# Kernel optimization log

Measured on AMD Instinct MI355X. Metric: run time of the kernel, lower is better.

## Reference

```python
import jax, jax.numpy as jnp
import numpy as np
import math

N = 8192
IN_FEATURES = 512
OUT_FEATURES = 64
NEG_INF = -9e15

def setup_inputs() -> dict:
    key = jax.random.key(0)
    k1, k2, k3, k4 = jax.random.split(key, 4)
    inp = jax.random.normal(k1, (N, IN_FEATURES), dtype=jnp.float32)
    adj = jax.random.randint(k2, (N, N), 0, 2, dtype=jnp.int32)
    # xavier_uniform with gain=1.414 for [in, out] weights
    limit = 1.414 * math.sqrt(6.0 / (IN_FEATURES + OUT_FEATURES))
    kW = jax.random.uniform(k3, (IN_FEATURES, OUT_FEATURES), dtype=jnp.float32, minval=-limit, maxval=limit)
    vW = jax.random.uniform(k4, (IN_FEATURES, OUT_FEATURES), dtype=jnp.float32, minval=-limit, maxval=limit)
    return {"input": inp, "adj": adj, "kW": kW, "vW": vW}

def reference(input, adj, kW, vW):
    kh = input @ kW                      # [N, d]
    vh = input @ vW                      # [N, d]
    d = kh.shape[1]
    K = (kh @ kh.T) / jnp.sqrt(jnp.asarray(d, dtype=kh.dtype))  # [N, N]
    scores = jnp.where(adj > 0, K, jnp.asarray(NEG_INF, dtype=K.dtype))
    attention = jax.nn.softmax(scores, axis=1)
    # dropout is a no-op (p=0.0 / eval mode)
    h_prime = attention @ vh             # [N, d]
    return jax.nn.elu(h_prime)           # concat=True path
```

## Files before the change

kernel.cpp:

```cpp
#include <hip/hip_runtime.h>
#include <math.h>

typedef __bf16 bf16_t;
typedef __bf16 bf16x8 __attribute__((ext_vector_type(8)));
typedef float f32x4 __attribute__((ext_vector_type(4)));

#define NN 8192
#define L2E 1.44269504088896340736f
#define SMAX 45.0f
#define KSCALE 0.35355339059327373f
#define ACCW 66

__global__ __launch_bounds__(256) void proj_kernel(
    const float* __restrict__ input,
    const float* __restrict__ kW,
    const float* __restrict__ vW,
    bf16_t* __restrict__ khs_hi,
    bf16_t* __restrict__ khs_lo,
    bf16_t* __restrict__ vhT)
{
    __shared__ __align__(16) bf16_t WkH[64][136];
    __shared__ __align__(16) bf16_t WkL[64][136];
    __shared__ __align__(16) bf16_t WvH[64][136];
    __shared__ __align__(16) bf16_t WvL[64][136];

    const int tid   = threadIdx.x;
    const int wv    = tid >> 6;
    const int lane  = tid & 63;
    const int l15   = lane & 15;
    const int quad  = lane >> 4;
    const int rbase = blockIdx.x * 64 + wv * 16;

    f32x4 kacc[4] = {};
    f32x4 vacc[4] = {};

    for (int kk = 0; kk < 4; ++kk) {
        __syncthreads();
        #pragma unroll
        for (int i = 0; i < 32; ++i) {
            int idx = tid + i * 256;
            int kl  = idx >> 6;
            int n   = idx & 63;
            float wk  = kW[(kk * 128 + kl) * 64 + n];
            float wv2 = vW[(kk * 128 + kl) * 64 + n];
            bf16_t kh = (bf16_t)wk;
            bf16_t vh = (bf16_t)wv2;
            WkH[n][kl] = kh;  WkL[n][kl] = (bf16_t)(wk - (float)kh);
            WvH[n][kl] = vh;  WvL[n][kl] = (bf16_t)(wv2 - (float)vh);
        }
        __syncthreads();

        #pragma unroll
        for (int kc = 0; kc < 4; ++kc) {
            const float* ap = &input[(size_t)(rbase + l15) * 512 + kk * 128 + kc * 32 + quad * 8];
            f32x4 a0 = *(const f32x4*)ap;
            f32x4 a1 = *(const f32x4*)(ap + 4);
            bf16x8 ah, al;
            #pragma unroll
            for (int j = 0; j < 4; ++j) {
                bf16_t h0 = (bf16_t)a0[j], h1 = (bf16_t)a1[j];
                ah[j]     = h0;  al[j]     = (bf16_t)(a0[j] - (float)h0);
                ah[4 + j] = h1;  al[4 + j] = (bf16_t)(a1[j] - (float)h1);
            }
            #pragma unroll
            for (int nb = 0; nb < 4; ++nb) {
                bf16x8 bkh = *(const bf16x8*)&WkH[nb * 16 + l15][kc * 32 + quad * 8];
                bf16x8 bkl = *(const bf16x8*)&WkL[nb * 16 + l15][kc * 32 + quad * 8];
                bf16x8 bvh = *(const bf16x8*)&WvH[nb * 16 + l15][kc * 32 + quad * 8];
                bf16x8 bvl = *(const bf16x8*)&WvL[nb * 16 + l15][kc * 32 + quad * 8];
                kacc[nb] = __builtin_amdgcn_mfma_f32_16x16x32_bf16(ah, bkh, kacc[nb], 0, 0, 0);
                kacc[nb] = __builtin_amdgcn_mfma_f32_16x16x32_bf16(al, bkh, kacc[nb], 0, 0, 0);
                kacc[nb] = __builtin_amdgcn_mfma_f32_16x16x32_bf16(ah, bkl, kacc[nb], 0, 0, 0);
                vacc[nb] = __builtin_amdgcn_mfma_f32_16x16x32_bf16(ah, bvh, vacc[nb], 0, 0, 0);
                vacc[nb] = __builtin_amdgcn_mfma_f32_16x16x32_bf16(al, bvh, vacc[nb], 0, 0, 0);
                vacc[nb] = __builtin_amdgcn_mfma_f32_16x16x32_bf16(ah, bvl, vacc[nb], 0, 0, 0);
            }
        }
    }

    #pragma unroll
    for (int nb = 0; nb < 4; ++nb) {
        const int dcol = nb * 16 + l15;
        #pragma unroll
        for (int r = 0; r < 4; ++r) {
            float v  = kacc[nb][r] * KSCALE;
            bf16_t h = (bf16_t)v;
            khs_hi[(size_t)(rbase + quad * 4 + r) * 64 + dcol] = h;
            khs_lo[(size_t)(rbase + quad * 4 + r) * 64 + dcol] = (bf16_t)(v - (float)h);
        }
        union { bf16_t b[4]; uint2 u; } pk;
        #pragma unroll
        for (int r = 0; r < 4; ++r) pk.b[r] = (bf16_t)vacc[nb][r];
        *(uint2*)&vhT[(size_t)dcol * NN + rbase + quad * 4] = pk.u;
    }
}

__global__ void zero_acc(float* __restrict__ acc) {
    int i = blockIdx.x * blockDim.x + threadIdx.x;
    if (i < NN * ACCW) acc[i] = 0.f;
}

__global__ __launch_bounds__(512, 4) void attn_kernel(
    const int* __restrict__ adj,
    const bf16_t* __restrict__ khs_hi,
    const bf16_t* __restrict__ khs_lo,
    const bf16_t* __restrict__ vhT,
    float* __restrict__ acc)
{
    __shared__ __align__(16) float PlBuf[8 * 1152];

    const int tid   = threadIdx.x;
    const int w     = tid >> 6;
    const int lane  = tid & 63;
    const int l15   = lane & 15;
    const int quad  = lane >> 4;
    const int rb    = blockIdx.x >> 1;
    const int ch    = blockIdx.x & 1;
    const int qbase = rb * 16;
    const int colstart = ch * 4096 + w * 512;

    const bf16x8 qh0 = *(const bf16x8*)&khs_hi[(size_t)(qbase + l15) * 64 + quad * 8];
    const bf16x8 qh1 = *(const bf16x8*)&khs_hi[(size_t)(qbase + l15) * 64 + 32 + quad * 8];
    const bf16x8 ql0 = *(const bf16x8*)&khs_lo[(size_t)(qbase + l15) * 64 + quad * 8];
    const bf16x8 ql1 = *(const bf16x8*)&khs_lo[(size_t)(qbase + l15) * 64 + 32 + quad * 8];

    bf16x8 ones;
    #pragma unroll
    for (int j = 0; j < 8; ++j) ones[j] = (bf16_t)1.0f;

    f32x4 o0 = {}, o1 = {}, o2 = {}, o3 = {}, o4 = {};

    const int* aptr = adj + (size_t)(qbase + quad * 4) * NN + colstart + l15;

    int acur[8], anxt[8];
    #pragma unroll
    for (int r = 0; r < 4; ++r) {
        acur[2 * r]     = aptr[(size_t)r * NN];
        acur[2 * r + 1] = aptr[(size_t)r * NN + 16];
    }

    for (int t = 0; t < 16; ++t) {
        const int colbase = colstart + t * 32;
        float* Plw = &PlBuf[w * 1152 + (t & 1) * 576];

        const bf16_t* kph = khs_hi + (size_t)(colbase + l15) * 64 + quad * 8;
        bf16x8 bh00 = *(const bf16x8*)(kph);
        bf16x8 bh01 = *(const bf16x8*)(kph + 32);
        bf16x8 bh10 = *(const bf16x8*)(kph + 16 * 64);
        bf16x8 bh11 = *(const bf16x8*)(kph + 16 * 64 + 32);
        const bf16_t* vp = vhT + (size_t)l15 * NN + colbase + quad * 8;
        bf16x8 bv0 = *(const bf16x8*)(vp);
        bf16x8 bv1 = *(const bf16x8*)(vp + (size_t)16 * NN);
        bf16x8 bv2 = *(const bf16x8*)(vp + (size_t)32 * NN);
        bf16x8 bv3 = *(const bf16x8*)(vp + (size_t)48 * NN);

        const int cnx = ((t + 1) & 15) * 32;
        #pragma unroll
        for (int r = 0; r < 4; ++r) {
            anxt[2 * r]     = aptr[(size_t)r * NN + cnx];
            anxt[2 * r + 1] = aptr[(size_t)r * NN + cnx + 16];
        }

        f32x4 zz = {};
        f32x4 s0 = __builtin_amdgcn_mfma_f32_16x16x32_bf16(qh0, bh00, zz, 0, 0, 0);
        s0 = __builtin_amdgcn_mfma_f32_16x16x32_bf16(qh1, bh01, s0, 0, 0, 0);
        s0 = __builtin_amdgcn_mfma_f32_16x16x32_bf16(ql0, bh00, s0, 0, 0, 0);
        s0 = __builtin_amdgcn_mfma_f32_16x16x32_bf16(ql1, bh01, s0, 0, 0, 0);
        f32x4 s1 = __builtin_amdgcn_mfma_f32_16x16x32_bf16(qh0, bh10, zz, 0, 0, 0);
        s1 = __builtin_amdgcn_mfma_f32_16x16x32_bf16(qh1, bh11, s1, 0, 0, 0);
        s1 = __builtin_amdgcn_mfma_f32_16x16x32_bf16(ql0, bh10, s1, 0, 0, 0);
        s1 = __builtin_amdgcn_mfma_f32_16x16x32_bf16(ql1, bh11, s1, 0, 0, 0);

        #pragma unroll
        for (int r = 0; r < 4; ++r) {
            float p0 = acur[2 * r]     > 0 ? __builtin_amdgcn_exp2f((s0[r] - SMAX) * L2E) : 0.f;
            float p1 = acur[2 * r + 1] > 0 ? __builtin_amdgcn_exp2f((s1[r] - SMAX) * L2E) : 0.f;
            Plw[(quad * 4 + r) * 36 + l15]      = p0;
            Plw[(quad * 4 + r) * 36 + 16 + l15] = p1;
        }

        __asm__ __volatile__("s_waitcnt lgkmcnt(0)" ::: "memory");

        f32x4 pfa = *(const f32x4*)&Plw[l15 * 36 + quad * 8];
        f32x4 pfb = *(const f32x4*)&Plw[l15 * 36 + quad * 8 + 4];
        bf16x8 pa;
        #pragma unroll
        for (int j = 0; j < 4; ++j) { pa[j] = (bf16_t)pfa[j]; pa[4 + j] = (bf16_t)pfb[j]; }

        o0 = __builtin_amdgcn_mfma_f32_16x16x32_bf16(pa, bv0, o0, 0, 0, 0);
        o1 = __builtin_amdgcn_mfma_f32_16x16x32_bf16(pa, bv1, o1, 0, 0, 0);
        o2 = __builtin_amdgcn_mfma_f32_16x16x32_bf16(pa, bv2, o2, 0, 0, 0);
        o3 = __builtin_amdgcn_mfma_f32_16x16x32_bf16(pa, bv3, o3, 0, 0, 0);
        o4 = __builtin_amdgcn_mfma_f32_16x16x32_bf16(pa, ones, o4, 0, 0, 0);

        #pragma unroll
        for (int i = 0; i < 8; ++i) acur[i] = anxt[i];
    }

    float* M = PlBuf;
    #pragma unroll
    for (int s = 4; s >= 1; s >>= 1) {
        __syncthreads();
        if (w >= s && w < 2 * s) {
            float* base = M + (w - s) * 16 * 68;
            #pragma unroll
            for (int r = 0; r < 4; ++r) {
                const int row = quad * 4 + r;
                base[row * 68 + l15]      = o0[r];
                base[row * 68 + 16 + l15] = o1[r];
                base[row * 68 + 32 + l15] = o2[r];
                base[row * 68 + 48 + l15] = o3[r];
                if (l15 == 0) base[row * 68 + 64] = o4[r];
            }
        }
        __syncthreads();
        if (w < s) {
            float* base = M + w * 16 * 68;
            #pragma unroll
            for (int r = 0; r < 4; ++r) {
                const int row = quad * 4 + r;
                o0[r] += base[row * 68 + l15];
                o1[r] += base[row * 68 + 16 + l15];
                o2[r] += base[row * 68 + 32 + l15];
                o3[r] += base[row * 68 + 48 + l15];
                o4[r] += base[row * 68 + 64];
            }
        }
    }

    if (w == 0) {
        #pragma unroll
        for (int r = 0; r < 4; ++r) {
            const size_t row = (size_t)qbase + quad * 4 + r;
            atomicAdd(&acc[row * ACCW + l15],      o0[r]);
            atomicAdd(&acc[row * ACCW + 16 + l15], o1[r]);
            atomicAdd(&acc[row * ACCW + 32 + l15], o2[r]);
            atomicAdd(&acc[row * ACCW + 48 + l15], o3[r]);
            if (l15 == 0) atomicAdd(&acc[row * ACCW + 64], o4[r]);
        }
    }
}

__global__ void finalize(const float* __restrict__ acc, float* __restrict__ out) {
    int i = blockIdx.x * blockDim.x + threadIdx.x;
    int row = i >> 6, d = i & 63;
    float l = acc[(size_t)row * ACCW + 64];
    float v = acc[(size_t)row * ACCW + d] / (l > 0.f ? l : 1.f);
    out[i] = v > 0.f ? v : expm1f(v);
}

extern "C" void kernel_launch(void* const* d_in, const int* in_sizes, int n_in,
                              void* d_out, int out_size, void* d_ws, size_t ws_size,
                              hipStream_t stream) {
    const float* input = nullptr;
    const int*   adj   = nullptr;
    const float* kW    = nullptr;
    const float* vW    = nullptr;
    for (int i = 0; i < n_in; ++i) {
        if (in_sizes[i] == 8192 * 512)            input = (const float*)d_in[i];
        else if (in_sizes[i] == 512 * 64) {
            if (!kW) kW = (const float*)d_in[i]; else vW = (const float*)d_in[i];
        } else                                    adj = (const int*)d_in[i];
    }
    float* out = (float*)d_out;

    bf16_t* khs_hi = (bf16_t*)d_ws;
    bf16_t* khs_lo = khs_hi + (size_t)NN * 64;
    bf16_t* vhT    = khs_lo + (size_t)NN * 64;
    float*  acc    = (float*)((char*)d_ws + 3u * 1024 * 1024);

    zero_acc<<<(NN * ACCW + 255) / 256, 256, 0, stream>>>(acc);
    proj_kernel<<<128, 256, 0, stream>>>(input, kW, vW, khs_hi, khs_lo, vhT);
    attn_kernel<<<1024, 512, 0, stream>>>(adj, khs_hi, khs_lo, vhT, acc);
    finalize<<<(NN * 64) / 512, 512, 0, stream>>>(acc, out);
}
```

Measured before the change: 519.1 us.

## Pre-pack adjacency into bitmask and read bits in attention kernel

Adds a bitpack kernel that streams the int32 adjacency matrix with coalesced loads and wave ballots into a 64-bit-per-64-column bitmask. The attention kernel then loads a few mask words per lane up front and distributes them by shuffle, instead of issuing strided int32 adjacency loads every tile. This aims to cut the memory traffic and load latency inside the attention loop. The cost is an extra kernel launch, a full pass over the adjacency matrix, and extra workspace for the mask.

```diff
diff --git a/kernel.cpp b/kernel.cpp
--- a/kernel.cpp
+++ b/kernel.cpp
@@ -95,13 +95,28 @@
     }
 }
 
+__global__ __launch_bounds__(256) void bitpack(
+    const int* __restrict__ adj, unsigned long long* __restrict__ mask64)
+{
+    const int gw   = (blockIdx.x * 256 + threadIdx.x) >> 6;
+    const int lane = threadIdx.x & 63;
+    const int* rp  = adj + (size_t)gw * NN + lane;
+    unsigned long long* mp = mask64 + (size_t)gw * 128;
+    #pragma unroll 8
+    for (int g = 0; g < 128; ++g) {
+        int v = rp[(size_t)g * 64];
+        unsigned long long b = __ballot(v > 0);
+        if (lane == 0) mp[g] = b;
+    }
+}
+
 __global__ void zero_acc(float* __restrict__ acc) {
     int i = blockIdx.x * blockDim.x + threadIdx.x;
     if (i < NN * ACCW) acc[i] = 0.f;
 }
 
 __global__ __launch_bounds__(512, 4) void attn_kernel(
-    const int* __restrict__ adj,
+    const unsigned int* __restrict__ mask,
     const bf16_t* __restrict__ khs_hi,
     const bf16_t* __restrict__ khs_lo,
     const bf16_t* __restrict__ vhT,
@@ -128,20 +143,24 @@
     #pragma unroll
     for (int j = 0; j < 8; ++j) ones[j] = (bf16_t)1.0f;
 
+    unsigned int mw[4];
+    {
+        const unsigned int* mp = mask + (size_t)(qbase + quad * 4) * 256 + ch * 128 + w * 16 + l15;
+        #pragma unroll
+        for (int r = 0; r < 4; ++r) mw[r] = mp[(size_t)r * 256];
+    }
+
     f32x4 o0 = {}, o1 = {}, o2 = {}, o3 = {}, o4 = {};
-
-    const int* aptr = adj + (size_t)(qbase + quad * 4) * NN + colstart + l15;
-
-    int acur[8], anxt[8];
-    #pragma unroll
-    for (int r = 0; r < 4; ++r) {
-        acur[2 * r]     = aptr[(size_t)r * NN];
-        acur[2 * r + 1] = aptr[(size_t)r * NN + 16];
-    }
 
     for (int t = 0; t < 16; ++t) {
         const int colbase = colstart + t * 32;
         float* Plw = &PlBuf[w * 1152 + (t & 1) * 576];
+
+        const int srcl = (lane & 48) | t;
+        unsigned int wr0 = __shfl(mw[0], srcl);
+        unsigned int wr1 = __shfl(mw[1], srcl);
+        unsigned int wr2 = __shfl(mw[2], srcl);
+        unsigned int wr3 = __shfl(mw[3], srcl);
 
         const bf16_t* kph = khs_hi + (size_t)(colbase + l15) * 64 + quad * 8;
         bf16x8 bh00 = *(const bf16x8*)(kph);
@@ -154,13 +173,6 @@
         bf16x8 bv2 = *(const bf16x8*)(vp + (size_t)32 * NN);
         bf16x8 bv3 = *(const bf16x8*)(vp + (size_t)48 * NN);
 
-        const int cnx = ((t + 1) & 15) * 32;
-        #pragma unroll
-        for (int r = 0; r < 4; ++r) {
-            anxt[2 * r]     = aptr[(size_t)r * NN + cnx];
-            anxt[2 * r + 1] = aptr[(size_t)r * NN + cnx + 16];
-        }
-
         f32x4 zz = {};
         f32x4 s0 = __builtin_amdgcn_mfma_f32_16x16x32_bf16(qh0, bh00, zz, 0, 0, 0);
         s0 = __builtin_amdgcn_mfma_f32_16x16x32_bf16(qh1, bh01, s0, 0, 0, 0);
@@ -171,10 +183,11 @@
         s1 = __builtin_amdgcn_mfma_f32_16x16x32_bf16(ql0, bh10, s1, 0, 0, 0);
         s1 = __builtin_amdgcn_mfma_f32_16x16x32_bf16(ql1, bh11, s1, 0, 0, 0);
 
+        unsigned int wrr[4] = { wr0, wr1, wr2, wr3 };
         #pragma unroll
         for (int r = 0; r < 4; ++r) {
-            float p0 = acur[2 * r]     > 0 ? __builtin_amdgcn_exp2f((s0[r] - SMAX) * L2E) : 0.f;
-            float p1 = acur[2 * r + 1] > 0 ? __builtin_amdgcn_exp2f((s1[r] - SMAX) * L2E) : 0.f;
+            float p0 = ((wrr[r] >> l15) & 1u)        ? __builtin_amdgcn_exp2f((s0[r] - SMAX) * L2E) : 0.f;
+            float p1 = ((wrr[r] >> (16 + l15)) & 1u) ? __builtin_amdgcn_exp2f((s1[r] - SMAX) * L2E) : 0.f;
             Plw[(quad * 4 + r) * 36 + l15]      = p0;
             Plw[(quad * 4 + r) * 36 + 16 + l15] = p1;
         }
@@ -192,9 +205,6 @@
         o2 = __builtin_amdgcn_mfma_f32_16x16x32_bf16(pa, bv2, o2, 0, 0, 0);
         o3 = __builtin_amdgcn_mfma_f32_16x16x32_bf16(pa, bv3, o3, 0, 0, 0);
         o4 = __builtin_amdgcn_mfma_f32_16x16x32_bf16(pa, ones, o4, 0, 0, 0);
-
-        #pragma unroll
-        for (int i = 0; i < 8; ++i) acur[i] = anxt[i];
     }
 
     float* M = PlBuf;
@@ -264,13 +274,16 @@
     }
     float* out = (float*)d_out;
 
-    bf16_t* khs_hi = (bf16_t*)d_ws;
-    bf16_t* khs_lo = khs_hi + (size_t)NN * 64;
-    bf16_t* vhT    = khs_lo + (size_t)NN * 64;
-    float*  acc    = (float*)((char*)d_ws + 3u * 1024 * 1024);
+    char* ws = (char*)d_ws;
+    bf16_t* khs_hi = (bf16_t*)ws;
+    bf16_t* khs_lo = (bf16_t*)(ws + 1u * 1024 * 1024);
+    bf16_t* vhT    = (bf16_t*)(ws + 2u * 1024 * 1024);
+    float*  acc    = (float*)(ws + 3u * 1024 * 1024);
+    unsigned long long* mask64 = (unsigned long long*)(ws + 6u * 1024 * 1024);
 
     zero_acc<<<(NN * ACCW + 255) / 256, 256, 0, stream>>>(acc);
     proj_kernel<<<128, 256, 0, stream>>>(input, kW, vW, khs_hi, khs_lo, vhT);
-    attn_kernel<<<1024, 512, 0, stream>>>(adj, khs_hi, khs_lo, vhT, acc);
+    bitpack<<<2048, 256, 0, stream>>>(adj, mask64);
+    attn_kernel<<<1024, 512, 0, stream>>>((const unsigned int*)mask64, khs_hi, khs_lo, vhT, acc);
     finalize<<<(NN * 64) / 512, 512, 0, stream>>>(acc, out);
 }
```

Measured after the change: 600.8 us. +15.7%, slower.
